# Performance work log

Hardware: AMD Instinct MI355X
Metric: run time of the kernel (lower is better)

Reference implementation:

```python
import jax, jax.numpy as jnp
import numpy as np

GROUPS = 8
HEADS = 4
EPS = 1e-5


def setup_inputs() -> dict:
    key = jax.random.key(0)
    ks = jax.random.split(key, 5)
    b, c, h, w = 4, 256, 64, 64
    x = jax.random.normal(ks[0], (b, c, h, w), dtype=jnp.float32)
    gn_w = jnp.ones((c,), dtype=jnp.float32)
    gn_b = jnp.zeros((c,), dtype=jnp.float32)
    qkv_w = jax.random.normal(ks[1], (3 * c, c), dtype=jnp.float32) * (c ** -0.5)
    qkv_b = jax.random.normal(ks[2], (3 * c,), dtype=jnp.float32) * 0.01
    proj_w = jax.random.normal(ks[3], (c, c), dtype=jnp.float32) * (c ** -0.5)
    proj_b = jax.random.normal(ks[4], (c,), dtype=jnp.float32) * 0.01
    return {"x": x, "gn_w": gn_w, "gn_b": gn_b, "qkv_w": qkv_w,
            "qkv_b": qkv_b, "proj_w": proj_w, "proj_b": proj_b}


def reference(x, gn_w, gn_b, qkv_w, qkv_b, proj_w, proj_b):
    b, c, h, w = x.shape
    head_dim = c // HEADS
    n = h * w

    # GroupNorm (biased variance, per torch)
    xg = x.reshape(b, GROUPS, c // GROUPS, h, w)
    mean = xg.mean(axis=(2, 3, 4), keepdims=True)
    var = xg.var(axis=(2, 3, 4), keepdims=True)
    xn = ((xg - mean) * jax.lax.rsqrt(var + EPS)).reshape(b, c, h, w)
    xn = xn * gn_w[None, :, None, None] + gn_b[None, :, None, None]

    # 1x1 conv qkv: [b,3c,h,w]
    qkv = jnp.einsum('oc,bchw->bohw', qkv_w, xn) + qkv_b[None, :, None, None]
    # split channel dim as (3, heads, head_dim), flatten spatial -> [b,3,H,d,n]
    qkv = qkv.reshape(b, 3, HEADS, head_dim, n)
    q, k, v = qkv[:, 0], qkv[:, 1], qkv[:, 2]  # each [b,H,d,n]

    scale = head_dim ** -0.5
    attn = jnp.einsum('bhci,bhcj->bhij', q, k) * scale  # [b,H,n,n]
    attn = jax.nn.softmax(attn, axis=-1)
    out = jnp.einsum('bhij,bhcj->bhci', attn, v)  # [b,H,d,n]
    out = out.reshape(b, c, h, w)

    out = jnp.einsum('oc,bchw->bohw', proj_w, out) + proj_b[None, :, None, None]
    return out + x
```

## Files before the change

### kernel.cpp

```cpp
#include <hip/hip_runtime.h>
#include <math.h>

#define NPIX 4096
#define CCH 256

typedef __attribute__((ext_vector_type(4))) float f32x4;
typedef __attribute__((ext_vector_type(8))) short s16x8;
typedef unsigned short u16;

__device__ __forceinline__ short bf16_rne(float x) {
  union { float f; unsigned u; } c; c.f = x;
  unsigned r = c.u + 0x7FFF + ((c.u >> 16) & 1);
  return (short)(r >> 16);
}
__device__ __forceinline__ unsigned cvtpk2(float lo, float hi) {
  unsigned r;
  asm("v_cvt_pk_bf16_f32 %0, %1, %2" : "=v"(r) : "v"(lo), "v"(hi));
  return r;
}
__device__ __forceinline__ unsigned pack2(float a, float b) {
  return cvtpk2(a, b);
}
__device__ __forceinline__ float max3f(float a, float b, float c) {
  float d;
  asm("v_max3_f32 %0, %1, %2, %3" : "=v"(d) : "v"(a), "v"(b), "v"(c));
  return d;
}
__device__ __forceinline__ float bf16_to_f32(unsigned short v) {
  return __uint_as_float(((unsigned)v) << 16);
}

__device__ __forceinline__ void plane32_swap(unsigned& a, unsigned& b) {
#if __has_builtin(__builtin_amdgcn_permlane32_swap)
  auto r = __builtin_amdgcn_permlane32_swap(a, b, false, false);
  a = r[0]; b = r[1];
#else
  asm("s_nop 2\n\tv_permlane32_swap_b32 %0, %1\n\ts_nop 2" : "+v"(a), "+v"(b));
#endif
}
__device__ __forceinline__ void plane16_swap(unsigned& a, unsigned& b) {
#if __has_builtin(__builtin_amdgcn_permlane16_swap)
  auto r = __builtin_amdgcn_permlane16_swap(a, b, false, false);
  a = r[0]; b = r[1];
#else
  asm("s_nop 2\n\tv_permlane16_swap_b32 %0, %1\n\ts_nop 2" : "+v"(a), "+v"(b));
#endif
}

__device__ __forceinline__ float red_max_cross(float x) {
  unsigned a = __float_as_uint(x), b = a;
  plane32_swap(a, b);
  float m = fmaxf(__uint_as_float(a), __uint_as_float(b));
  a = __float_as_uint(m); b = a;
  plane16_swap(a, b);
  return fmaxf(__uint_as_float(a), __uint_as_float(b));
}
__device__ __forceinline__ float red_sum_cross(float x) {
  unsigned a = __float_as_uint(x), b = a;
  plane32_swap(a, b);
  float m = __uint_as_float(a) + __uint_as_float(b);
  a = __float_as_uint(m); b = a;
  plane16_swap(a, b);
  return __uint_as_float(a) + __uint_as_float(b);
}

#define QSCALE 0.18033688011f

__global__ __launch_bounds__(256) void gn_stats_part(
    const float* __restrict__ x, double2* __restrict__ partials)
{
  const int blk = blockIdx.x;
  const int bg = blk >> 3, chunk = blk & 7;
  const float4* base = (const float4*)(x + (size_t)bg * 131072 + (size_t)chunk * 16384);
  double s = 0.0, ss = 0.0;
  for (int idx = threadIdx.x; idx < 4096; idx += 256) {
    float4 v = base[idx];
    s  += (double)v.x + (double)v.y + (double)v.z + (double)v.w;
    ss += (double)v.x * v.x + (double)v.y * v.y + (double)v.z * v.z + (double)v.w * v.w;
  }
  __shared__ double rs[256], rss[256];
  rs[threadIdx.x] = s; rss[threadIdx.x] = ss;
  __syncthreads();
  for (int off = 128; off > 0; off >>= 1) {
    if (threadIdx.x < off) { rs[threadIdx.x] += rs[threadIdx.x + off]; rss[threadIdx.x] += rss[threadIdx.x + off]; }
    __syncthreads();
  }
  if (threadIdx.x == 0) {
    double2 p; p.x = rs[0]; p.y = rss[0];
    partials[blk] = p;
  }
}

__global__ __launch_bounds__(256) void wcvt_kernel(
    const float* __restrict__ qkv_w, const float* __restrict__ proj_w, const float* __restrict__ qkv_b,
    const double2* __restrict__ partials, const float* __restrict__ gn_w, const float* __restrict__ gn_b,
    u16* __restrict__ wq, u16* __restrict__ wp, float* __restrict__ biasq,
    float* __restrict__ alpha, float* __restrict__ beta)
{
  int idx = blockIdx.x * 256 + threadIdx.x;
  if (idx < 196608) {
    float v = qkv_w[idx];
    if (idx < 65536) v *= QSCALE;
    wq[idx] = (u16)bf16_rne(v);
  } else {
    int j = idx - 196608;
    wp[j] = (u16)bf16_rne(proj_w[j]);
  }
  if (idx < 768) {
    float bv = qkv_b[idx];
    if (idx < 256) bv *= QSCALE;
    biasq[idx] = bv;
  }
  if (blockIdx.x == 0) {
    __shared__ float sm[32], sr[32];
    const int tid = threadIdx.x;
    if (tid < 32) {
      double s = 0.0, ss = 0.0;
      for (int c = 0; c < 8; ++c) { double2 p = partials[tid * 8 + c]; s += p.x; ss += p.y; }
      double mean = s / 131072.0;
      double var  = ss / 131072.0 - mean * mean;
      sm[tid] = (float)mean;
      sr[tid] = (float)(1.0 / sqrt(var + 1e-5));
    }
    __syncthreads();
#pragma unroll
    for (int p = 0; p < 4; ++p) {
      int e = p * 256 + tid;
      int ch = e & 255;
      int bg = (e >> 8) * 8 + (ch >> 5);
      float a = sr[bg] * gn_w[ch];
      alpha[e] = a;
      beta[e]  = gn_b[ch] - sm[bg] * a;
    }
  }
}

__global__ __launch_bounds__(256) void gn_apply_t_kernel(
    const float* __restrict__ x, const float* __restrict__ alpha, const float* __restrict__ beta,
    u16* __restrict__ Xt)
{
  const int b = blockIdx.z, c0 = blockIdx.y * 64, n0 = blockIdx.x * 64;
  const int tid = threadIdx.x;
  __shared__ u16 T[64 * 68];
  const int n4 = (tid & 15) * 4, cr = tid >> 4;
#pragma unroll
  for (int p = 0; p < 4; ++p) {
    int cl = cr + 16 * p;
    int c = c0 + cl;
    float a = alpha[b * CCH + c], bt = beta[b * CCH + c];
    float4 v = *(const float4*)&x[((size_t)b * CCH + c) * NPIX + n0 + n4];
    T[(n4 + 0) * 68 + cl] = (u16)bf16_rne(v.x * a + bt);
    T[(n4 + 1) * 68 + cl] = (u16)bf16_rne(v.y * a + bt);
    T[(n4 + 2) * 68 + cl] = (u16)bf16_rne(v.z * a + bt);
    T[(n4 + 3) * 68 + cl] = (u16)bf16_rne(v.w * a + bt);
  }
  __syncthreads();
#pragma unroll
  for (int it = 0; it < 2; ++it) {
    int linear = it * 256 + tid;
    int n = linear >> 3, ch = linear & 7;
    s16x8 v = *(const s16x8*)&T[n * 68 + ch * 8];
    *(s16x8*)&Xt[((size_t)b * NPIX + n0 + n) * CCH + c0 + ch * 8] = v;
  }
}

__global__ __launch_bounds__(256) void qkv_gemm_kernel(
    const u16* __restrict__ Wbf, const float* __restrict__ biasv, const u16* __restrict__ Xt,
    u16* __restrict__ Qt, u16* __restrict__ Kt, u16* __restrict__ Vb)
{
  const int nblk = blockIdx.x, m0 = blockIdx.y * 64;
  const int tid = threadIdx.x, wave = tid >> 6, lane = tid & 63;
  const int n16 = lane & 15, quad = lane >> 4;
  const int n0 = nblk * 128 + wave * 32;

  f32x4 acc[4][2];
#pragma unroll
  for (int a = 0; a < 4; ++a)
#pragma unroll
    for (int c = 0; c < 2; ++c) acc[a][c] = (f32x4){0.f, 0.f, 0.f, 0.f};

#pragma unroll
  for (int k0 = 0; k0 < 256; k0 += 32) {
    s16x8 af[4], bfr[2];
#pragma unroll
    for (int msub = 0; msub < 4; ++msub)
      af[msub] = *(const s16x8*)&Wbf[(size_t)(m0 + msub * 16 + n16) * 256 + k0 + quad * 8];
#pragma unroll
    for (int nsub = 0; nsub < 2; ++nsub)
      bfr[nsub] = *(const s16x8*)&Xt[(size_t)(n0 + nsub * 16 + n16) * 256 + k0 + quad * 8];
#pragma unroll
    for (int msub = 0; msub < 4; ++msub)
#pragma unroll
      for (int nsub = 0; nsub < 2; ++nsub)
        acc[msub][nsub] = __builtin_amdgcn_mfma_f32_16x16x32_bf16(af[msub], bfr[nsub], acc[msub][nsub], 0, 0, 0);
  }

  __shared__ u16 T[8704];
  if (m0 < 512) {
#pragma unroll
    for (int msub = 0; msub < 4; ++msub)
#pragma unroll
      for (int nsub = 0; nsub < 2; ++nsub) {
        float b0 = biasv[m0 + msub * 16 + quad * 4 + 0];
        float b1 = biasv[m0 + msub * 16 + quad * 4 + 1];
        float b2 = biasv[m0 + msub * 16 + quad * 4 + 2];
        float b3 = biasv[m0 + msub * 16 + quad * 4 + 3];
        uint2 w2;
        w2.x = pack2(acc[msub][nsub][0] + b0, acc[msub][nsub][1] + b1);
        w2.y = pack2(acc[msub][nsub][2] + b2, acc[msub][nsub][3] + b3);
        *(uint2*)&T[(wave * 32 + nsub * 16 + n16) * 68 + msub * 16 + quad * 4] = w2;
      }
    __syncthreads();
    u16* dst = (m0 < 256) ? Qt : Kt;
    const int coff = m0 & 255;
#pragma unroll
    for (int it = 0; it < 4; ++it) {
      int linear = it * 256 + tid;
      int n = linear >> 3, ch = linear & 7;
      s16x8 v = *(const s16x8*)&T[n * 68 + ch * 8];
      *(s16x8*)&dst[(size_t)(nblk * 128 + n) * 256 + coff + ch * 8] = v;
    }
  } else {
#pragma unroll
    for (int msub = 0; msub < 4; ++msub)
#pragma unroll
      for (int nsub = 0; nsub < 2; ++nsub) {
        int ncol = wave * 32 + nsub * 16 + n16;
#pragma unroll
        for (int r = 0; r < 4; ++r) {
          int m = msub * 16 + quad * 4 + r;
          T[m * 136 + ncol] = (u16)bf16_rne(acc[msub][nsub][r] + biasv[m0 + m]);
        }
      }
    __syncthreads();
    const int b = (nblk * 128) >> 12, i0n = (nblk * 128) & 4095;
#pragma unroll
    for (int it = 0; it < 4; ++it) {
      int linear = it * 256 + tid;
      int mloc = linear >> 4, ch = linear & 15;
      s16x8 v = *(const s16x8*)&T[mloc * 136 + ch * 8];
      int c = (m0 - 512) + mloc;
      *(s16x8*)&Vb[((size_t)b * CCH + c) * NPIX + i0n + ch * 8] = v;
    }
  }
}

__device__ __forceinline__ void kv_load(
    const u16* __restrict__ Kb, const u16* __restrict__ Vg, int h, int j0, int sj, int part,
    s16x8& k0, s16x8& k1, s16x8& v0, s16x8& v1)
{
  const s16x8* kp = (const s16x8*)&Kb[(size_t)(j0 + sj) * 256 + h * 64 + part * 16];
  const s16x8* vp = (const s16x8*)&Vg[(size_t)sj * NPIX + j0 + part * 16];
  k0 = kp[0]; k1 = kp[1]; v0 = vp[0]; v1 = vp[1];
}
__device__ __forceinline__ void kv_store(
    u16* Ksb, u16* Vsb, int sbase, int rr0,
    s16x8 k0, s16x8 k1, s16x8 v0, s16x8 v1)
{
  *(s16x8*)&Ksb[sbase + (rr0 + 0) * 128] = k0;
  *(s16x8*)&Ksb[sbase + (rr0 + 1) * 128] = k1;
  *(s16x8*)&Vsb[sbase + (rr0 + 0) * 128] = v0;
  *(s16x8*)&Vsb[sbase + (rr0 + 1) * 128] = v1;
}

__device__ __forceinline__ void attn_tile(
    const u16* Ksb, const u16* Vsb, const s16x8 qf[2], int lane,
    f32x4 ot[4], float& m_i, float& l_i)
{
  f32x4 st[4];
#pragma unroll
  for (int a = 0; a < 4; ++a) st[a] = (f32x4){0.f, 0.f, 0.f, 0.f};
  __builtin_amdgcn_s_setprio(1);
#pragma unroll
  for (int ks = 0; ks < 2; ++ks)
#pragma unroll
    for (int jsub = 0; jsub < 4; ++jsub) {
      s16x8 a = *(const s16x8*)&Ksb[(jsub * 2 + ks) * 520 + lane * 8];
      st[jsub] = __builtin_amdgcn_mfma_f32_16x16x32_bf16(a, qf[ks], st[jsub], 0, 0, 0);
    }
  __builtin_amdgcn_s_setprio(0);

  float m0 = max3f(st[0][0], st[0][1], st[0][2]);
  float m1 = max3f(st[0][3], st[1][0], st[1][1]);
  float m2 = max3f(st[1][2], st[1][3], st[2][0]);
  float m3 = max3f(st[2][1], st[2][2], st[2][3]);
  float m4 = max3f(st[3][0], st[3][1], st[3][2]);
  float m5 = max3f(m0, m1, st[3][3]);
  float m6 = max3f(m2, m3, m4);
  float tm = fmaxf(m5, m6);
  tm = red_max_cross(tm);

  if (__any(tm > m_i + 8.0f)) {
    float mn = fmaxf(m_i, tm);
    float al = __builtin_amdgcn_exp2f(m_i - mn);
    m_i = mn;
    l_i *= al;
#pragma unroll
    for (int dsub = 0; dsub < 4; ++dsub)
#pragma unroll
      for (int r = 0; r < 4; ++r) ot[dsub][r] *= al;
  }

#pragma unroll
  for (int jsub = 0; jsub < 4; ++jsub)
#pragma unroll
    for (int r = 0; r < 4; ++r)
      st[jsub][r] = __builtin_amdgcn_exp2f(st[jsub][r] - m_i);

  float s0 = (st[0][0] + st[0][1]) + (st[0][2] + st[0][3]);
  float s1 = (st[1][0] + st[1][1]) + (st[1][2] + st[1][3]);
  float s2 = (st[2][0] + st[2][1]) + (st[2][2] + st[2][3]);
  float s3 = (st[3][0] + st[3][1]) + (st[3][2] + st[3][3]);
  float ps = (s0 + s1) + (s2 + s3);
  ps = red_sum_cross(ps);
  l_i += ps;

  s16x8 pb[2];
#pragma unroll
  for (int ks = 0; ks < 2; ++ks) {
    unsigned a0 = cvtpk2(st[2 * ks][0], st[2 * ks][1]);
    unsigned a1 = cvtpk2(st[2 * ks][2], st[2 * ks][3]);
    unsigned b0 = cvtpk2(st[2 * ks + 1][0], st[2 * ks + 1][1]);
    unsigned b1 = cvtpk2(st[2 * ks + 1][2], st[2 * ks + 1][3]);
    plane32_swap(a0, b0);
    plane16_swap(a0, b0);
    plane32_swap(a1, b1);
    plane16_swap(a1, b1);
    union { unsigned u[4]; s16x8 v; } pu;
    pu.u[0] = a0; pu.u[1] = a1; pu.u[2] = b0; pu.u[3] = b1;
    pb[ks] = pu.v;
  }

  __builtin_amdgcn_s_setprio(1);
#pragma unroll
  for (int ks = 0; ks < 2; ++ks)
#pragma unroll
    for (int dsub = 0; dsub < 4; ++dsub) {
      s16x8 a = *(const s16x8*)&Vsb[(dsub * 2 + ks) * 520 + lane * 8];
      ot[dsub] = __builtin_amdgcn_mfma_f32_16x16x32_bf16(a, pb[ks], ot[dsub], 0, 0, 0);
    }
  __builtin_amdgcn_s_setprio(0);
}

__global__ __launch_bounds__(256, 8) void attn_kernel5(
    const u16* __restrict__ Qt, const u16* __restrict__ Kt,
    const u16* __restrict__ Vb, u16* __restrict__ P0, u16* __restrict__ P1,
    float* __restrict__ mlbuf)
{
  const int b = blockIdx.z, h = blockIdx.y;
  const int xb = blockIdx.x;
  const int half = xb >> 6, iblk = xb & 63;
  const int tid = threadIdx.x;
  const int wave = tid >> 6, lane = tid & 63;
  const int n16 = lane & 15, quad = lane >> 4;
  const int i0w = iblk * 64 + wave * 16;

  __shared__ u16 Ks[8 * 520];
  __shared__ u16 Vs[8 * 520];

  const u16* Qb = Qt + (size_t)b * NPIX * 256;
  const u16* Kb = Kt + (size_t)b * NPIX * 256;
  const u16* Vg = Vb + ((size_t)b * CCH + h * 64) * NPIX;

  s16x8 qf[2];
#pragma unroll
  for (int ks = 0; ks < 2; ++ks)
    qf[ks] = *(const s16x8*)&Qb[(size_t)(i0w + n16) * 256 + h * 64 + ks * 32 + quad * 8];

  f32x4 ot[4];
#pragma unroll
  for (int a = 0; a < 4; ++a) ot[a] = (f32x4){0.f, 0.f, 0.f, 0.f};
  float m_i = -1e30f;
  float l_i = 0.f;

  const int sj = tid >> 2;
  const int part = tid & 3;
  const int sh = part >> 1;
  const int rr0 = (part & 1) * 2;
  const int sbase = ((sj >> 4) * 2 + sh) * 520 + (sj & 15) * 8;
  const int jbase = half * 2048;

  s16x8 k0, k1, v0, v1;

#pragma unroll 1
  for (int t = 0; t < 32; ++t) {
    kv_load(Kb, Vg, h, jbase + t * 64, sj, part, k0, k1, v0, v1);
    __syncthreads();
    kv_store(Ks, Vs, sbase, rr0, k0, k1, v0, v1);
    __syncthreads();
    attn_tile(Ks, Vs, qf, lane, ot, m_i, l_i);
  }

  float rl = 1.0f / l_i;
  u16* dst = (half == 0) ? P0 : P1;
#pragma unroll
  for (int dsub = 0; dsub < 4; ++dsub) {
    uint2 w2;
    w2.x = cvtpk2(ot[dsub][0] * rl, ot[dsub][1] * rl);
    w2.y = cvtpk2(ot[dsub][2] * rl, ot[dsub][3] * rl);
    size_t addr = (size_t)((size_t)b * NPIX + i0w + n16) * 256 + h * 64 + dsub * 16 + quad * 4;
    *(uint2*)&dst[addr] = w2;
  }
  if (quad == 0) {
    int idx = half * 65536 + b * 16384 + h * 4096 + i0w + n16;
    float2 ml; ml.x = m_i; ml.y = l_i;
    *(float2*)&mlbuf[idx * 2] = ml;
  }
}

__global__ __launch_bounds__(256) void combine_kernel(
    const u16* __restrict__ P0, u16* __restrict__ Ot, const float* __restrict__ mlbuf)
{
  const int t = threadIdx.x;
  const int r = blockIdx.x * 32 + (t >> 3);
  const int seg = t & 7;
  const int b = r >> 12, i = r & 4095;
  const int h = seg >> 1;
  const int idx = b * 16384 + h * 4096 + i;
  float2 ml0 = *(const float2*)&mlbuf[(size_t)idx * 2];
  float2 ml1 = *(const float2*)&mlbuf[(size_t)(65536 + idx) * 2];
  float m = fmaxf(ml0.x, ml1.x);
  float c0 = ml0.y * __builtin_amdgcn_exp2f(ml0.x - m);
  float c1 = ml1.y * __builtin_amdgcn_exp2f(ml1.x - m);
  float rn = 1.0f / (c0 + c1);
  float w0 = c0 * rn, w1 = c1 * rn;
  size_t base = (size_t)r * 256 + seg * 32;
#pragma unroll
  for (int p = 0; p < 4; ++p) {
    s16x8 a = *(const s16x8*)&P0[base + p * 8];
    s16x8 c = *(const s16x8*)&Ot[base + p * 8];
    union { unsigned u[4]; s16x8 v; } o;
#pragma unroll
    for (int e = 0; e < 4; ++e) {
      float lo = w0 * bf16_to_f32((unsigned short)a[2 * e])     + w1 * bf16_to_f32((unsigned short)c[2 * e]);
      float hi = w0 * bf16_to_f32((unsigned short)a[2 * e + 1]) + w1 * bf16_to_f32((unsigned short)c[2 * e + 1]);
      o.u[e] = cvtpk2(lo, hi);
    }
    *(s16x8*)&Ot[base + p * 8] = o.v;
  }
}

__global__ __launch_bounds__(256) void proj_gemm_kernel(
    const u16* __restrict__ Wp, const float* __restrict__ proj_b, const u16* __restrict__ Ot,
    const float* __restrict__ x, float* __restrict__ out)
{
  const int nblk = blockIdx.x, m0 = blockIdx.y * 64;
  const int tid = threadIdx.x, wave = tid >> 6, lane = tid & 63;
  const int n16 = lane & 15, quad = lane >> 4;
  const int n0 = nblk * 128 + wave * 32;

  f32x4 acc[4][2];
#pragma unroll
  for (int a = 0; a < 4; ++a)
#pragma unroll
    for (int c = 0; c < 2; ++c) acc[a][c] = (f32x4){0.f, 0.f, 0.f, 0.f};

#pragma unroll
  for (int k0 = 0; k0 < 256; k0 += 32) {
    s16x8 af[4], bfr[2];
#pragma unroll
    for (int msub = 0; msub < 4; ++msub)
      af[msub] = *(const s16x8*)&Wp[(size_t)(m0 + msub * 16 + n16) * 256 + k0 + quad * 8];
#pragma unroll
    for (int nsub = 0; nsub < 2; ++nsub)
      bfr[nsub] = *(const s16x8*)&Ot[(size_t)(n0 + nsub * 16 + n16) * 256 + k0 + quad * 8];
#pragma unroll
    for (int msub = 0; msub < 4; ++msub)
#pragma unroll
      for (int nsub = 0; nsub < 2; ++nsub)
        acc[msub][nsub] = __builtin_amdgcn_mfma_f32_16x16x32_bf16(af[msub], bfr[nsub], acc[msub][nsub], 0, 0, 0);
  }

  __shared__ float T[64 * 132];
#pragma unroll
  for (int msub = 0; msub < 4; ++msub)
#pragma unroll
    for (int nsub = 0; nsub < 2; ++nsub) {
      int ncol = wave * 32 + nsub * 16 + n16;
#pragma unroll
      for (int r = 0; r < 4; ++r) {
        int m = msub * 16 + quad * 4 + r;
        T[m * 132 + ncol] = acc[msub][nsub][r];
      }
    }
  __syncthreads();
  const int b = (nblk * 128) >> 12, i0n = (nblk * 128) & 4095;
#pragma unroll
  for (int it = 0; it < 8; ++it) {
    int linear = it * 256 + tid;
    int m = linear >> 5, ch = linear & 31;
    f32x4 v = *(const f32x4*)&T[m * 132 + ch * 4];
    float bs = proj_b[m0 + m];
    size_t g = ((size_t)b * CCH + m0 + m) * NPIX + i0n + ch * 4;
    float4 rv = *(const float4*)&x[g];
    float4 o;
    o.x = v[0] + bs + rv.x; o.y = v[1] + bs + rv.y;
    o.z = v[2] + bs + rv.z; o.w = v[3] + bs + rv.w;
    *(float4*)&out[g] = o;
  }
}

extern "C" void kernel_launch(void* const* d_in, const int* in_sizes, int n_in,
                              void* d_out, int out_size, void* d_ws, size_t ws_size,
                              hipStream_t stream)
{
  const float* x      = (const float*)d_in[0];
  const float* gn_w   = (const float*)d_in[1];
  const float* gn_b   = (const float*)d_in[2];
  const float* qkv_w  = (const float*)d_in[3];
  const float* qkv_b  = (const float*)d_in[4];
  const float* proj_w = (const float*)d_in[5];
  const float* proj_b = (const float*)d_in[6];
  float* out = (float*)d_out;

  float* ws    = (float*)d_ws;
  float* alpha = ws;
  float* beta  = ws + 1024;
  float* biasq = ws + 2048;
  double2* partials = (double2*)(ws + 2816);
  u16*   wq    = (u16*)(ws + 4096);
  u16*   wp    = (u16*)(ws + 102400);
  u16*   Xt    = (u16*)(ws + 135168);
  u16*   Qt    = (u16*)(ws + 2232320);
  u16*   Kt    = (u16*)(ws + 4329472);
  u16*   Vb    = (u16*)(ws + 6426624);
  u16*   Ot    = (u16*)(ws + 8523776);
  float* mlbuf = ws + 10620928;

  u16* P0 = Xt;

  gn_stats_part<<<256, 256, 0, stream>>>(x, partials);
  wcvt_kernel<<<1024, 256, 0, stream>>>(qkv_w, proj_w, qkv_b, partials, gn_w, gn_b,
                                        wq, wp, biasq, alpha, beta);
  gn_apply_t_kernel<<<dim3(64, 4, 4), 256, 0, stream>>>(x, alpha, beta, Xt);
  qkv_gemm_kernel<<<dim3(128, 12), 256, 0, stream>>>(wq, biasq, Xt, Qt, Kt, Vb);
  attn_kernel5<<<dim3(128, 4, 4), 256, 0, stream>>>(Qt, Kt, Vb, P0, Ot, mlbuf);
  combine_kernel<<<512, 256, 0, stream>>>(P0, Ot, mlbuf);
  proj_gemm_kernel<<<dim3(128, 4), 256, 0, stream>>>(wp, proj_b, Ot, x, out);
}
```

Baseline: 257.5 us.

## Switch attention to 32x32x16 MFMA with 32 query rows per wave and double-buffered LDS

Rewrites the attention kernel to use 32x32x16 bf16 MFMA tiles, so each wave handles 32 query rows instead of 16 and the grid is halved. K/V tiles are double-buffered in shared memory, so the global load of the next tile overlaps the compute on the current one and only one barrier is needed per tile. The cross-lane reductions and P repacking now need only permlane32 swaps. The larger accumulators raise register pressure, and occupancy drops to 4 blocks per CU.

```diff
diff --git a/kernel.cpp b/kernel.cpp
--- a/kernel.cpp
+++ b/kernel.cpp
@@ -5,6 +5,7 @@
 #define CCH 256
 
 typedef __attribute__((ext_vector_type(4))) float f32x4;
+typedef __attribute__((ext_vector_type(16))) float f32x16;
 typedef __attribute__((ext_vector_type(8))) short s16x8;
 typedef unsigned short u16;
 
@@ -38,29 +39,14 @@
   asm("s_nop 2\n\tv_permlane32_swap_b32 %0, %1\n\ts_nop 2" : "+v"(a), "+v"(b));
 #endif
 }
-__device__ __forceinline__ void plane16_swap(unsigned& a, unsigned& b) {
-#if __has_builtin(__builtin_amdgcn_permlane16_swap)
-  auto r = __builtin_amdgcn_permlane16_swap(a, b, false, false);
-  a = r[0]; b = r[1];
-#else
-  asm("s_nop 2\n\tv_permlane16_swap_b32 %0, %1\n\ts_nop 2" : "+v"(a), "+v"(b));
-#endif
-}
-
-__device__ __forceinline__ float red_max_cross(float x) {
+__device__ __forceinline__ float red_max_half(float x) {
   unsigned a = __float_as_uint(x), b = a;
   plane32_swap(a, b);
-  float m = fmaxf(__uint_as_float(a), __uint_as_float(b));
-  a = __float_as_uint(m); b = a;
-  plane16_swap(a, b);
   return fmaxf(__uint_as_float(a), __uint_as_float(b));
 }
-__device__ __forceinline__ float red_sum_cross(float x) {
+__device__ __forceinline__ float red_sum_half(float x) {
   unsigned a = __float_as_uint(x), b = a;
   plane32_swap(a, b);
-  float m = __uint_as_float(a) + __uint_as_float(b);
-  a = __float_as_uint(m); b = a;
-  plane16_swap(a, b);
   return __uint_as_float(a) + __uint_as_float(b);
 }
 
@@ -245,7 +231,7 @@
   }
 }
 
-__device__ __forceinline__ void kv_load(
+__device__ __forceinline__ void kv_load6(
     const u16* __restrict__ Kb, const u16* __restrict__ Vg, int h, int j0, int sj, int part,
     s16x8& k0, s16x8& k1, s16x8& v0, s16x8& v1)
 {
@@ -253,42 +239,50 @@
   const s16x8* vp = (const s16x8*)&Vg[(size_t)sj * NPIX + j0 + part * 16];
   k0 = kp[0]; k1 = kp[1]; v0 = vp[0]; v1 = vp[1];
 }
-__device__ __forceinline__ void kv_store(
-    u16* Ksb, u16* Vsb, int sbase, int rr0,
+__device__ __forceinline__ void kv_store6(
+    u16* Ksb, u16* Vsb, int sbase,
     s16x8 k0, s16x8 k1, s16x8 v0, s16x8 v1)
 {
-  *(s16x8*)&Ksb[sbase + (rr0 + 0) * 128] = k0;
-  *(s16x8*)&Ksb[sbase + (rr0 + 1) * 128] = k1;
-  *(s16x8*)&Vsb[sbase + (rr0 + 0) * 128] = v0;
-  *(s16x8*)&Vsb[sbase + (rr0 + 1) * 128] = v1;
-}
-
-__device__ __forceinline__ void attn_tile(
-    const u16* Ksb, const u16* Vsb, const s16x8 qf[2], int lane,
-    f32x4 ot[4], float& m_i, float& l_i)
-{
-  f32x4 st[4];
-#pragma unroll
-  for (int a = 0; a < 4; ++a) st[a] = (f32x4){0.f, 0.f, 0.f, 0.f};
+  *(s16x8*)&Ksb[sbase]       = k0;
+  *(s16x8*)&Ksb[sbase + 256] = k1;
+  *(s16x8*)&Vsb[sbase]       = v0;
+  *(s16x8*)&Vsb[sbase + 256] = v1;
+}
+
+__device__ __forceinline__ void attn_tile6(
+    const u16* Ksb, const u16* Vsb, const s16x8 qf[4], int lane,
+    f32x16 ot[2], float& m_i, float& l_i)
+{
+  f32x16 st[2];
+#pragma unroll
+  for (int r = 0; r < 16; ++r) { st[0][r] = 0.f; st[1][r] = 0.f; }
+
   __builtin_amdgcn_s_setprio(1);
 #pragma unroll
-  for (int ks = 0; ks < 2; ++ks)
-#pragma unroll
-    for (int jsub = 0; jsub < 4; ++jsub) {
-      s16x8 a = *(const s16x8*)&Ksb[(jsub * 2 + ks) * 520 + lane * 8];
-      st[jsub] = __builtin_amdgcn_mfma_f32_16x16x32_bf16(a, qf[ks], st[jsub], 0, 0, 0);
+  for (int kq = 0; kq < 4; ++kq)
+#pragma unroll
+    for (int jsub = 0; jsub < 2; ++jsub) {
+      s16x8 a = *(const s16x8*)&Ksb[(jsub * 4 + kq) * 512 + lane * 8];
+      st[jsub] = __builtin_amdgcn_mfma_f32_32x32x16_bf16(a, qf[kq], st[jsub], 0, 0, 0);
     }
   __builtin_amdgcn_s_setprio(0);
 
-  float m0 = max3f(st[0][0], st[0][1], st[0][2]);
-  float m1 = max3f(st[0][3], st[1][0], st[1][1]);
-  float m2 = max3f(st[1][2], st[1][3], st[2][0]);
-  float m3 = max3f(st[2][1], st[2][2], st[2][3]);
-  float m4 = max3f(st[3][0], st[3][1], st[3][2]);
-  float m5 = max3f(m0, m1, st[3][3]);
-  float m6 = max3f(m2, m3, m4);
-  float tm = fmaxf(m5, m6);
-  tm = red_max_cross(tm);
+  float c0 = max3f(st[0][0],  st[0][1],  st[0][2]);
+  float c1 = max3f(st[0][3],  st[0][4],  st[0][5]);
+  float c2 = max3f(st[0][6],  st[0][7],  st[0][8]);
+  float c3 = max3f(st[0][9],  st[0][10], st[0][11]);
+  float c4 = max3f(st[0][12], st[0][13], st[0][14]);
+  float c5 = max3f(st[0][15], st[1][0],  st[1][1]);
+  float c6 = max3f(st[1][2],  st[1][3],  st[1][4]);
+  float c7 = max3f(st[1][5],  st[1][6],  st[1][7]);
+  float c8 = max3f(st[1][8],  st[1][9],  st[1][10]);
+  float c9 = max3f(st[1][11], st[1][12], st[1][13]);
+  float d0 = max3f(c0, c1, c2);
+  float d1 = max3f(c3, c4, c5);
+  float d2 = max3f(c6, c7, c8);
+  float d3 = max3f(c9, st[1][14], st[1][15]);
+  float tm = fmaxf(fmaxf(d0, d1), fmaxf(d2, d3));
+  tm = red_max_half(tm);
 
   if (__any(tm > m_i + 8.0f)) {
     float mn = fmaxf(m_i, tm);
@@ -296,113 +290,122 @@
     m_i = mn;
     l_i *= al;
 #pragma unroll
-    for (int dsub = 0; dsub < 4; ++dsub)
-#pragma unroll
-      for (int r = 0; r < 4; ++r) ot[dsub][r] *= al;
-  }
-
-#pragma unroll
-  for (int jsub = 0; jsub < 4; ++jsub)
-#pragma unroll
-    for (int r = 0; r < 4; ++r)
-      st[jsub][r] = __builtin_amdgcn_exp2f(st[jsub][r] - m_i);
-
-  float s0 = (st[0][0] + st[0][1]) + (st[0][2] + st[0][3]);
-  float s1 = (st[1][0] + st[1][1]) + (st[1][2] + st[1][3]);
-  float s2 = (st[2][0] + st[2][1]) + (st[2][2] + st[2][3]);
-  float s3 = (st[3][0] + st[3][1]) + (st[3][2] + st[3][3]);
-  float ps = (s0 + s1) + (s2 + s3);
-  ps = red_sum_cross(ps);
+    for (int r = 0; r < 16; ++r) { ot[0][r] *= al; ot[1][r] *= al; }
+  }
+
+#pragma unroll
+  for (int f = 0; f < 2; ++f)
+#pragma unroll
+    for (int r = 0; r < 16; ++r)
+      st[f][r] = __builtin_amdgcn_exp2f(st[f][r] - m_i);
+
+  float s0 = (st[0][0] + st[0][1]) + (st[0][2]  + st[0][3]);
+  float s1 = (st[0][4] + st[0][5]) + (st[0][6]  + st[0][7]);
+  float s2 = (st[0][8] + st[0][9]) + (st[0][10] + st[0][11]);
+  float s3 = (st[0][12]+ st[0][13])+ (st[0][14] + st[0][15]);
+  float s4 = (st[1][0] + st[1][1]) + (st[1][2]  + st[1][3]);
+  float s5 = (st[1][4] + st[1][5]) + (st[1][6]  + st[1][7]);
+  float s6 = (st[1][8] + st[1][9]) + (st[1][10] + st[1][11]);
+  float s7 = (st[1][12]+ st[1][13])+ (st[1][14] + st[1][15]);
+  float ps = ((s0 + s1) + (s2 + s3)) + ((s4 + s5) + (s6 + s7));
+  ps = red_sum_half(ps);
   l_i += ps;
 
-  s16x8 pb[2];
-#pragma unroll
-  for (int ks = 0; ks < 2; ++ks) {
-    unsigned a0 = cvtpk2(st[2 * ks][0], st[2 * ks][1]);
-    unsigned a1 = cvtpk2(st[2 * ks][2], st[2 * ks][3]);
-    unsigned b0 = cvtpk2(st[2 * ks + 1][0], st[2 * ks + 1][1]);
-    unsigned b1 = cvtpk2(st[2 * ks + 1][2], st[2 * ks + 1][3]);
-    plane32_swap(a0, b0);
-    plane16_swap(a0, b0);
-    plane32_swap(a1, b1);
-    plane16_swap(a1, b1);
+#pragma unroll
+  for (int jq = 0; jq < 4; ++jq) {
+    const int jsub = jq >> 1;
+    const int b0 = (jq & 1) * 8;
+    const int b1 = b0 + 4;
+    unsigned u0 = cvtpk2(st[jsub][b0 + 0], st[jsub][b0 + 1]);
+    unsigned u1 = cvtpk2(st[jsub][b0 + 2], st[jsub][b0 + 3]);
+    unsigned u2 = cvtpk2(st[jsub][b1 + 0], st[jsub][b1 + 1]);
+    unsigned u3 = cvtpk2(st[jsub][b1 + 2], st[jsub][b1 + 3]);
+    plane32_swap(u0, u2);
+    plane32_swap(u1, u3);
     union { unsigned u[4]; s16x8 v; } pu;
-    pu.u[0] = a0; pu.u[1] = a1; pu.u[2] = b0; pu.u[3] = b1;
-    pb[ks] = pu.v;
-  }
-
-  __builtin_amdgcn_s_setprio(1);
-#pragma unroll
-  for (int ks = 0; ks < 2; ++ks)
-#pragma unroll
-    for (int dsub = 0; dsub < 4; ++dsub) {
-      s16x8 a = *(const s16x8*)&Vsb[(dsub * 2 + ks) * 520 + lane * 8];
-      ot[dsub] = __builtin_amdgcn_mfma_f32_16x16x32_bf16(a, pb[ks], ot[dsub], 0, 0, 0);
-    }
-  __builtin_amdgcn_s_setprio(0);
-}
-
-__global__ __launch_bounds__(256, 8) void attn_kernel5(
+    pu.u[0] = u0; pu.u[1] = u1; pu.u[2] = u2; pu.u[3] = u3;
+    __builtin_amdgcn_s_setprio(1);
+#pragma unroll
+    for (int dsub = 0; dsub < 2; ++dsub) {
+      s16x8 a = *(const s16x8*)&Vsb[(dsub * 4 + jq) * 512 + lane * 8];
+      ot[dsub] = __builtin_amdgcn_mfma_f32_32x32x16_bf16(a, pu.v, ot[dsub], 0, 0, 0);
+    }
+    __builtin_amdgcn_s_setprio(0);
+  }
+}
+
+__global__ __launch_bounds__(256, 4) void attn_kernel6(
     const u16* __restrict__ Qt, const u16* __restrict__ Kt,
     const u16* __restrict__ Vb, u16* __restrict__ P0, u16* __restrict__ P1,
     float* __restrict__ mlbuf)
 {
   const int b = blockIdx.z, h = blockIdx.y;
   const int xb = blockIdx.x;
-  const int half = xb >> 6, iblk = xb & 63;
+  const int half = xb >> 5, iblk = xb & 31;
   const int tid = threadIdx.x;
   const int wave = tid >> 6, lane = tid & 63;
-  const int n16 = lane & 15, quad = lane >> 4;
-  const int i0w = iblk * 64 + wave * 16;
-
-  __shared__ u16 Ks[8 * 520];
-  __shared__ u16 Vs[8 * 520];
+  const int i0w = iblk * 128 + wave * 32;
+
+  __shared__ u16 Ks[2][4096];
+  __shared__ u16 Vs[2][4096];
 
   const u16* Qb = Qt + (size_t)b * NPIX * 256;
   const u16* Kb = Kt + (size_t)b * NPIX * 256;
   const u16* Vg = Vb + ((size_t)b * CCH + h * 64) * NPIX;
 
-  s16x8 qf[2];
-#pragma unroll
-  for (int ks = 0; ks < 2; ++ks)
-    qf[ks] = *(const s16x8*)&Qb[(size_t)(i0w + n16) * 256 + h * 64 + ks * 32 + quad * 8];
-
-  f32x4 ot[4];
-#pragma unroll
-  for (int a = 0; a < 4; ++a) ot[a] = (f32x4){0.f, 0.f, 0.f, 0.f};
+  s16x8 qf[4];
+#pragma unroll
+  for (int kq = 0; kq < 4; ++kq)
+    qf[kq] = *(const s16x8*)&Qb[(size_t)(i0w + (lane & 31)) * 256 + h * 64 + kq * 16 + (lane >> 5) * 8];
+
+  f32x16 ot[2];
+#pragma unroll
+  for (int r = 0; r < 16; ++r) { ot[0][r] = 0.f; ot[1][r] = 0.f; }
   float m_i = -1e30f;
   float l_i = 0.f;
 
   const int sj = tid >> 2;
   const int part = tid & 3;
-  const int sh = part >> 1;
-  const int rr0 = (part & 1) * 2;
-  const int sbase = ((sj >> 4) * 2 + sh) * 520 + (sj & 15) * 8;
+  const int sbase = ((sj >> 5) * 4 + part) * 512 + (sj & 31) * 8;
   const int jbase = half * 2048;
 
   s16x8 k0, k1, v0, v1;
 
+  kv_load6(Kb, Vg, h, jbase, sj, part, k0, k1, v0, v1);
+  kv_store6(Ks[0], Vs[0], sbase, k0, k1, v0, v1);
+  __syncthreads();
+
 #pragma unroll 1
-  for (int t = 0; t < 32; ++t) {
-    kv_load(Kb, Vg, h, jbase + t * 64, sj, part, k0, k1, v0, v1);
+  for (int t = 0; t < 30; t += 2) {
+    kv_load6(Kb, Vg, h, jbase + (t + 1) * 64, sj, part, k0, k1, v0, v1);
+    attn_tile6(Ks[0], Vs[0], qf, lane, ot, m_i, l_i);
+    kv_store6(Ks[1], Vs[1], sbase, k0, k1, v0, v1);
     __syncthreads();
-    kv_store(Ks, Vs, sbase, rr0, k0, k1, v0, v1);
+    kv_load6(Kb, Vg, h, jbase + (t + 2) * 64, sj, part, k0, k1, v0, v1);
+    attn_tile6(Ks[1], Vs[1], qf, lane, ot, m_i, l_i);
+    kv_store6(Ks[0], Vs[0], sbase, k0, k1, v0, v1);
     __syncthreads();
-    attn_tile(Ks, Vs, qf, lane, ot, m_i, l_i);
-  }
+  }
+  kv_load6(Kb, Vg, h, jbase + 31 * 64, sj, part, k0, k1, v0, v1);
+  attn_tile6(Ks[0], Vs[0], qf, lane, ot, m_i, l_i);
+  kv_store6(Ks[1], Vs[1], sbase, k0, k1, v0, v1);
+  __syncthreads();
+  attn_tile6(Ks[1], Vs[1], qf, lane, ot, m_i, l_i);
 
   float rl = 1.0f / l_i;
   u16* dst = (half == 0) ? P0 : P1;
-#pragma unroll
-  for (int dsub = 0; dsub < 4; ++dsub) {
-    uint2 w2;
-    w2.x = cvtpk2(ot[dsub][0] * rl, ot[dsub][1] * rl);
-    w2.y = cvtpk2(ot[dsub][2] * rl, ot[dsub][3] * rl);
-    size_t addr = (size_t)((size_t)b * NPIX + i0w + n16) * 256 + h * 64 + dsub * 16 + quad * 4;
-    *(uint2*)&dst[addr] = w2;
-  }
-  if (quad == 0) {
-    int idx = half * 65536 + b * 16384 + h * 4096 + i0w + n16;
+  const size_t rowbase = (size_t)((size_t)b * NPIX + i0w + (lane & 31)) * 256 + h * 64 + (lane >> 5) * 4;
+#pragma unroll
+  for (int dsub = 0; dsub < 2; ++dsub)
+#pragma unroll
+    for (int q = 0; q < 4; ++q) {
+      uint2 w2;
+      w2.x = cvtpk2(ot[dsub][4 * q + 0] * rl, ot[dsub][4 * q + 1] * rl);
+      w2.y = cvtpk2(ot[dsub][4 * q + 2] * rl, ot[dsub][4 * q + 3] * rl);
+      *(uint2*)&dst[rowbase + dsub * 32 + q * 8] = w2;
+    }
+  if (lane < 32) {
+    int idx = half * 65536 + b * 16384 + h * 4096 + i0w + lane;
     float2 ml; ml.x = m_i; ml.y = l_i;
     *(float2*)&mlbuf[idx * 2] = ml;
   }
@@ -534,7 +537,7 @@
                                         wq, wp, biasq, alpha, beta);
   gn_apply_t_kernel<<<dim3(64, 4, 4), 256, 0, stream>>>(x, alpha, beta, Xt);
   qkv_gemm_kernel<<<dim3(128, 12), 256, 0, stream>>>(wq, biasq, Xt, Qt, Kt, Vb);
-  attn_kernel5<<<dim3(128, 4, 4), 256, 0, stream>>>(Qt, Kt, Vb, P0, Ot, mlbuf);
+  attn_kernel6<<<dim3(64, 4, 4), 256, 0, stream>>>(Qt, Kt, Vb, P0, Ot, mlbuf);
   combine_kernel<<<512, 256, 0, stream>>>(P0, Ot, mlbuf);
   proj_gemm_kernel<<<dim3(128, 4), 256, 0, stream>>>(wp, proj_b, Ot, x, out);
 }
```

New measurement: 237.0 us. 8.0% less time.
